# Performance work log

Measured on AMD Instinct MI355X. Metric: run time of the kernel, lower is better.

## Reference

```python
import jax, jax.numpy as jnp
import numpy as np

B, S, H = 2, 4096, 2048          # batch, seq_len, hidden_size
NH, D, W = 8, 128, 4             # num_kv_heads, head_dim, conv_kernel_size (window)
KD = NH * D                      # key_dim == value_dim == 1024
ROPE_BASE = 1000000.0
EPS = 1e-6


def _rope_tables(d, end, base):
    inv = 1.0 / (base ** (np.arange(0, d, 2)[: d // 2].astype(np.float32) / d))
    f = np.outer(np.arange(end, dtype=np.float32), inv)  # [end, d/2]
    return jnp.asarray(np.cos(f)), jnp.asarray(np.sin(f))


def _apply_rope(x, cos, sin):
    # x: [B,S,h,d]; llama-style interleaved pairs (2i, 2i+1)
    x0, x1 = x[..., 0::2], x[..., 1::2]
    c = cos[None, :, None, :]
    s = sin[None, :, None, :]
    o0 = x0 * c - x1 * s
    o1 = x0 * s + x1 * c
    return jnp.stack([o0, o1], axis=-1).reshape(x.shape)


def setup_inputs() -> dict:
    key = jax.random.key(0)
    ks = jax.random.split(key, 7)
    sd = lambda k, shape, fan_in: jax.random.normal(k, shape, jnp.float32) * (fan_in ** -0.5)
    return {
        "x": jax.random.normal(ks[0], (B, S, H), jnp.float32),
        "W_qkv": sd(ks[1], (H, 3 * KD), H),
        "W_z": sd(ks[2], (H, KD), H),
        "W_b": sd(ks[3], (H, NH), H),
        "W_a": sd(ks[4], (H, NH), H),
        "norm_w": jnp.ones((KD,), jnp.float32),
        "W_out": sd(ks[5], (KD, H), KD),
    }


def _forward(x, W_qkv, W_z, W_b, W_a, norm_w, W_out):
    cos, sin = _rope_tables(D, S, ROPE_BASE)
    qkv = x @ W_qkv
    q, k, v = qkv[..., :KD], qkv[..., KD:2 * KD], qkv[..., 2 * KD:]
    z = x @ W_z           # [B,S,KD]
    bg = x @ W_b          # [B,S,NH]
    ag = x @ W_a          # [B,S,NH]

    q4 = _apply_rope(q.reshape(B, S, NH, D), cos, sin)
    k4 = _apply_rope(k.reshape(B, S, NH, D), cos, sin)
    v4 = v.reshape(B, S, NH, D)

    # Windowed gated delta rule: out[i] = sum_{j=i-W..i} (q_i.k_j/sqrt(D)) * sigmoid(a_i*b_j) * v_j
    # Implemented per diagonal offset (W+1 small, fixed) -- never materializes an SxS matrix.
    scale = 1.0 / np.sqrt(D).astype(np.float32)
    out = jnp.zeros_like(v4)
    idx = jnp.arange(S)
    for off in range(W + 1):
        if off == 0:
            kj, vj, bj = k4, v4, bg
        else:
            kj = jnp.pad(k4, ((0, 0), (off, 0), (0, 0), (0, 0)))[:, :S]
            vj = jnp.pad(v4, ((0, 0), (off, 0), (0, 0), (0, 0)))[:, :S]
            bj = jnp.pad(bg, ((0, 0), (off, 0), (0, 0)))[:, :S]
        score = jnp.einsum('bshd,bshd->bsh', q4, kj) * scale
        s = score * jax.nn.sigmoid(ag * bj)
        s = jnp.where((idx >= off)[None, :, None], s, 0.0)
        out = out + s[..., None] * vj
    # position 0 bypasses the attention entirely: output[0] = v[0]
    out = out.at[:, 0].set(v4[:, 0])

    y = out.reshape(B, S, KD) * jax.nn.sigmoid(z)
    # GatedRMSNorm(y, z): rmsnorm(y) * weight * silu(z)
    yf = y.reshape(B * S, KD)
    zf = z.reshape(B * S, KD)
    rms = jnp.sqrt(jnp.mean(yf * yf, axis=-1, keepdims=True) + EPS)
    yn = (yf / rms) * norm_w * (zf * jax.nn.sigmoid(zf))
    return yn.reshape(B, S, KD) @ W_out


def reference(x, W_qkv, W_z, W_b, W_a, norm_w, W_out):
    return _forward(x, W_qkv, W_z, W_b, W_a, norm_w, W_out)
```

## Files before the change

kernel.cpp:

```cpp
#include <hip/hip_runtime.h>
#include <hip/hip_bf16.h>
#include <stdint.h>

#define B_   2
#define S_   4096
#define H_   2048
#define NH_  8
#define D_   128
#define KD_  1024
#define MR   (B_ * S_)
#define NQKVZ 4096

typedef __attribute__((ext_vector_type(8))) short bf16x8;
typedef __attribute__((ext_vector_type(4))) float f32x4;

__device__ __forceinline__ short f2bf(float f) {
    union { float f; uint32_t u; } v; v.f = f;
    uint32_t r = v.u + 0x7FFF + ((v.u >> 16) & 1);
    return (short)(r >> 16);
}
__device__ __forceinline__ float bf2f(unsigned short u) {
    union { uint32_t u; float f; } v; v.u = (uint32_t)u << 16; return v.f;
}

__device__ __forceinline__ void async_ld16(const void* g, void* l) {
    __builtin_amdgcn_global_load_lds(
        (const __attribute__((address_space(1))) uint32_t*)g,
        (__attribute__((address_space(3))) uint32_t*)l, 16, 0, 0);
}

__global__ __launch_bounds__(256) void k_wba(const float* __restrict__ Wb,
                                             const float* __restrict__ Wa,
                                             float* __restrict__ Wba) {
    int idx = blockIdx.x * 256 + threadIdx.x;
    int k = idx & 2047, c = idx >> 11;
    float v = (c < 8) ? Wb[(size_t)k * 8 + c] : Wa[(size_t)k * 8 + (c - 8)];
    Wba[(size_t)c * 2048 + k] = v;
}

__global__ __launch_bounds__(256) void k_cvt_bgag4(const float* __restrict__ x,
                                                   short* __restrict__ xb,
                                                   const float* __restrict__ Wba,
                                                   float* __restrict__ bgag) {
    const int m0 = blockIdx.x * 4, t = threadIdx.x;
    __shared__ float xs[4][2048];
    __shared__ float part[4][256];
#pragma unroll
    for (int rr = 0; rr < 4; rr++) {
        const float4* xr = (const float4*)(x + (size_t)(m0 + rr) * H_);
        float4 a = xr[t], b = xr[t + 256];
        ((float4*)xs[rr])[t] = a;
        ((float4*)xs[rr])[t + 256] = b;
        short4 oa, ob;
        oa.x = f2bf(a.x); oa.y = f2bf(a.y); oa.z = f2bf(a.z); oa.w = f2bf(a.w);
        ob.x = f2bf(b.x); ob.y = f2bf(b.y); ob.z = f2bf(b.z); ob.w = f2bf(b.w);
        short4* xo = (short4*)(xb + (size_t)(m0 + rr) * H_);
        xo[t] = oa;
        xo[t + 256] = ob;
    }
    __syncthreads();
    const int c = t & 15, seg = t >> 4;
    const int kb = seg * 128;
    const float4* W4 = (const float4*)(Wba + (size_t)c * 2048 + kb);
    const float4* x0 = (const float4*)&xs[0][kb];
    const float4* x1 = (const float4*)&xs[1][kb];
    const float4* x2 = (const float4*)&xs[2][kb];
    const float4* x3 = (const float4*)&xs[3][kb];
    float a0 = 0.f, a1 = 0.f, a2 = 0.f, a3 = 0.f;
#pragma unroll 8
    for (int k4 = 0; k4 < 32; k4++) {
        float4 w = W4[k4];
        float4 v0 = x0[k4], v1 = x1[k4], v2 = x2[k4], v3 = x3[k4];
        a0 += w.x * v0.x + w.y * v0.y + w.z * v0.z + w.w * v0.w;
        a1 += w.x * v1.x + w.y * v1.y + w.z * v1.z + w.w * v1.w;
        a2 += w.x * v2.x + w.y * v2.y + w.z * v2.z + w.w * v2.w;
        a3 += w.x * v3.x + w.y * v3.y + w.z * v3.z + w.w * v3.w;
    }
    part[0][t] = a0; part[1][t] = a1; part[2][t] = a2; part[3][t] = a3;
    __syncthreads();
    if (t < 64) {
        int rr = t >> 4, cc = t & 15;
        float s = 0.f;
#pragma unroll
        for (int j = 0; j < 16; j++) s += part[rr][j * 16 + cc];
        bgag[(size_t)(m0 + rr) * 16 + cc] = s;
    }
}

__global__ __launch_bounds__(256) void k_transpose_cvt(const float* __restrict__ W,
                                                       short* __restrict__ Wt,
                                                       int K, int N) {
    __shared__ float tile[32][33];
    int n0 = blockIdx.x * 32, k0 = blockIdx.y * 32;
    int tx = threadIdx.x, ty = threadIdx.y;
#pragma unroll
    for (int i = 0; i < 32; i += 8)
        tile[ty + i][tx] = W[(size_t)(k0 + ty + i) * N + n0 + tx];
    __syncthreads();
#pragma unroll
    for (int i = 0; i < 32; i += 8)
        Wt[(size_t)(n0 + ty + i) * K + k0 + tx] = f2bf(tile[tx][ty + i]);
}

__global__ __launch_bounds__(256) void k_ropetab(float2* __restrict__ ctab) {
    int idx = blockIdx.x * 256 + threadIdx.x;
    int i = idx & 63, s = idx >> 6;
    float inv = exp2f(-(float)i * (2.0f / 128.0f) * 19.931568569324174f);
    float f = (float)s * inv;
    float sn, cs;
    sincosf(f, &sn, &cs);
    ctab[idx] = make_float2(cs, sn);
}

#define PHASE_TAIL() \
    __builtin_amdgcn_s_setprio(0); \
    asm volatile("s_waitcnt vmcnt(%0)" :: "n"(2 + LB) : "memory"); \
    asm volatile("s_barrier" ::: "memory")
#define LDB_P(SET, BASE, KH) \
    _Pragma("unroll") for (int j = 0; j < NF; j++) \
        bf##SET[j] = *(const bf16x8*)((BASE) + 2 * AHB + (KH) * BHB + (wn + j * 16 + mrow) * 64 + kcA)
#define LDA03_P(SET, BASE, KH) \
    _Pragma("unroll") for (int i = 0; i < 4; i++) \
        af##SET[i] = *(const bf16x8*)((BASE) + (KH) * AHB + (wm + i * 16 + mrow) * 64 + kcA)
#define LDA47_S(BASE, KH) \
    _Pragma("unroll") for (int i = 0; i < 4; i++) \
        afS[i] = *(const bf16x8*)((BASE) + (KH) * AHB + (wm + 64 + i * 16 + mrow) * 64 + kcA)
#define MFMA_PH(SET) \
    _Pragma("unroll") for (int i = 0; i < 4; i++) \
    _Pragma("unroll") for (int j = 0; j < NF; j++) \
        acc[i][j] = __builtin_amdgcn_mfma_f32_16x16x32_bf16(af##SET[i], bf##SET[j], acc[i][j], 0, 0, 0); \
    _Pragma("unroll") for (int i = 0; i < 4; i++) \
    _Pragma("unroll") for (int j = 0; j < NF; j++) \
        acc[4 + i][j] = __builtin_amdgcn_mfma_f32_16x16x32_bf16(afS[i], bf##SET[j], acc[4 + i][j], 0, 0, 0)

template <int BN, int EPI>
__global__ __launch_bounds__(512, 2) void k_gemm256(const short* __restrict__ A,
                                                    const short* __restrict__ Bt,
                                                    float* __restrict__ Cf,
                                                    unsigned short* __restrict__ Cb,
                                                    const float2* __restrict__ ctab,
                                                    int M, int N, int K) {
    constexpr int BM = 256;
    constexpr int NF = BN / 64;
    constexpr int LB = BN / 128;
    constexpr int AHB = BM * 64;
    constexpr int BHB = BN * 64;
    constexpr int BUFB = 2 * AHB + 2 * BHB;
    constexpr int LDSB = (EPI == 0) ? 133120 : 2 * BUFB;
    __shared__ __align__(16) char lds[LDSB];

    const int t = threadIdx.x;
    const int lane = t & 63, wave = t >> 6;
    const int mrow = lane & 15;
    const int kcA = (((lane >> 4) ^ ((mrow >> 1) & 3)) * 16);

    const int nwg = gridDim.x;
    const int w0 = blockIdx.x;
    const int wg = (w0 & 7) * (nwg >> 3) + (w0 >> 3);
    const int NB = N / BN;
    const int bn = (wg % NB) * BN;
    const int bm = (wg / NB) * BM;

    const int wm = (wave >> 2) * 128;
    const int wn = (wave & 3) * (BN / 4);

    const short* __restrict__ Ab = A + (size_t)bm * K;
    const short* __restrict__ Bb = Bt + (size_t)bn * K;

    int aoff[2], adst[2];
#pragma unroll
    for (int l = 0; l < 2; l++) {
        int c = t + l * 512;
        int row = c >> 2;
        int kcg = (c & 3) ^ ((row >> 1) & 3);
        aoff[l] = row * K + kcg * 8;
        adst[l] = c * 16;
    }
    int boff[LB], bdst[LB];
#pragma unroll
    for (int l = 0; l < LB; l++) {
        int c = t + l * 512;
        int row = c >> 2;
        int kcg = (c & 3) ^ ((row >> 1) & 3);
        boff[l] = row * K + kcg * 8;
        bdst[l] = c * 16;
    }

    const int NT = K >> 6;

    auto stageA = [&](int kt, int kh, int p) {
        const short* g = Ab + kt * 64 + kh * 32;
        char* d = lds + p * BUFB + kh * AHB;
#pragma unroll
        for (int l = 0; l < 2; l++) async_ld16(g + aoff[l], d + adst[l]);
    };
    auto stageB = [&](int kt, int kh, int p) {
        const short* g = Bb + kt * 64 + kh * 32;
        char* d = lds + p * BUFB + 2 * AHB + kh * BHB;
#pragma unroll
        for (int l = 0; l < LB; l++) async_ld16(g + boff[l], d + bdst[l]);
    };

    f32x4 acc[8][NF] = {};
    bf16x8 afE[4], bfE[NF], afO[4], bfO[NF], afS[4];

    stageA(0, 0, 0); stageB(0, 0, 0);
    stageA(0, 1, 0); stageB(0, 1, 0);
    {
        int k1 = (NT > 1) ? 1 : 0;
        stageA(k1, 0, 1); stageB(k1, 0, 1);
    }
    asm volatile("s_waitcnt vmcnt(%0)" :: "n"(2 * (2 + LB)) : "memory");
    asm volatile("s_barrier" ::: "memory");
    LDB_P(E, lds, 0); LDA03_P(E, lds, 0);
    asm volatile("s_waitcnt vmcnt(%0)" :: "n"(2 + LB) : "memory");
    asm volatile("s_barrier" ::: "memory");

    for (int kt = 0; kt < NT; kt++) {
        const int p = kt & 1;
        const char* base = lds + p * BUFB;
        const char* baseN = lds + (p ^ 1) * BUFB;
        const int k1 = (kt + 1 < NT) ? (kt + 1) : (NT - 1);
        const int k2 = (kt + 2 < NT) ? (kt + 2) : (NT - 1);

        LDA47_S(base, 0);
        LDB_P(O, base, 1); LDA03_P(O, base, 1);
        stageA(k1, 1, p ^ 1); stageB(k1, 1, p ^ 1);
        __builtin_amdgcn_sched_barrier(0);
        __builtin_amdgcn_s_setprio(1);
        MFMA_PH(E);
        PHASE_TAIL();

        LDA47_S(base, 1);
        LDB_P(E, baseN, 0); LDA03_P(E, baseN, 0);
        stageA(k2, 0, p); stageB(k2, 0, p);
        __builtin_amdgcn_sched_barrier(0);
        __builtin_amdgcn_s_setprio(1);
        MFMA_PH(O);
        PHASE_TAIL();
    }
    asm volatile("s_waitcnt vmcnt(0)" ::: "memory");

    const int crow = (lane >> 4) * 4, ccol = lane & 15;
    if (EPI == 0) {
        float* lf = (float*)lds;
#pragma unroll
        for (int p2 = 0; p2 < 2; p2++) {
            __syncthreads();
#pragma unroll
            for (int i = 0; i < 4; i++) {
                const int ii = p2 * 4 + i;
#pragma unroll
                for (int j = 0; j < NF; j++)
#pragma unroll
                    for (int r = 0; r < 4; r++) {
                        int rl = wm + ii * 16 + crow + r;
                        int slot = (rl & 63) | ((rl >> 7) << 6);
                        lf[slot * 260 + wn + j * 16 + ccol] = acc[ii][j][r];
                    }
            }
            __syncthreads();
#pragma unroll
            for (int rep = 0; rep < 16; rep++) {
                int idx = rep * 512 + t;
                int slot = idx >> 6, c4 = idx & 63;
                int rl = (slot & 63) + p2 * 64 + ((slot >> 6) << 7);
                float4 v = *(const float4*)&lf[slot * 260 + c4 * 4];
                *(float4*)(Cf + (size_t)(bm + rl) * N + bn + c4 * 4) = v;
            }
        }
    } else {
#pragma unroll
        for (int i = 0; i < 8; i++)
#pragma unroll
            for (int j = 0; j < NF; j++) {
                const int col = bn + wn + j * 16 + ccol;
                const int rowb = bm + wm + i * 16 + crow;
                const bool qk = col < 2048;
                const int fi = (col & 127) >> 1;
                const bool even = (col & 1) == 0;
                uint32_t* Cd = (uint32_t*)(Cb + ((size_t)rowb * N + (col & ~1)));
#pragma unroll
                for (int r = 0; r < 4; r++) {
                    float v = acc[i][j][r];
                    if (qk) {
                        int s = (rowb + r) & (S_ - 1);
                        float2 cs = ctab[s * 64 + fi];
                        float pp = __shfl_xor(v, 1);
                        v = even ? v * cs.x - pp * cs.y : v * cs.x + pp * cs.y;
                    }
                    int hb = (int)(unsigned short)f2bf(v);
                    int pb = __shfl_xor(hb, 1);
                    if (even)
                        Cd[(size_t)r * (N >> 1)] = (uint32_t)(hb | (pb << 16));
                }
            }
    }
}

__global__ __launch_bounds__(256) void k_attn4(const unsigned short* __restrict__ qkvz,
                                               const float* __restrict__ bgag,
                                               const float* __restrict__ norm_w,
                                               short* __restrict__ yn) {
    const int m0 = blockIdx.x * 4;
    const int s0 = m0 & (S_ - 1);
    const int t = threadIdx.x;
    __shared__ unsigned short kvls[8][2048];
    __shared__ float sc[4][NH_][5];
    __shared__ float red[4][4];

#pragma unroll
    for (int i = 0; i < 8; i++) {
        int g = m0 - 4 + i;
        g = (g < 0) ? 0 : g;
        const uint4* src = (const uint4*)(qkvz + (size_t)g * NQKVZ + 1024);
        ((uint4*)kvls[i])[t] = src[t];
    }
    __syncthreads();

    {
        const int r = t >> 6, h = (t >> 3) & 7, l8 = t & 7;
        const int sr = s0 + r;
        const int nOff = (sr < 4 ? sr : 4) + 1;
        float qv[16];
        {
            const unsigned short* qg = qkvz + (size_t)(m0 + r) * NQKVZ + h * 128 + l8 * 16;
#pragma unroll
            for (int d = 0; d < 16; d++) qv[d] = bf2f(qg[d]);
        }
        const float ag = bgag[(size_t)(m0 + r) * 16 + 8 + h];
#pragma unroll
        for (int off = 0; off < 5; off++) {
            float acc = 0.f;
            const unsigned short* kk = kvls[r + 4 - off] + h * 128 + l8 * 16;
#pragma unroll
            for (int d = 0; d < 16; d++) acc += qv[d] * bf2f(kk[d]);
#pragma unroll
            for (int w = 1; w < 8; w <<= 1) acc += __shfl_xor(acc, w);
            if (l8 == 0) {
                float val = 0.f;
                if (off < nOff) {
                    float bg = bgag[(size_t)(m0 + r - off) * 16 + h];
                    float g = 1.f / (1.f + expf(-ag * bg));
                    val = acc * 0.08838834764831845f * g;
                }
                sc[r][h][off] = val;
            }
        }
    }
    __syncthreads();

    const int e0 = t * 4, h2 = t >> 5;
    float yv[4][4], zs[4][4], ssr[4];
    float nw[4];
    {
        const float4 n4 = *(const float4*)(norm_w + e0);
        nw[0] = n4.x; nw[1] = n4.y; nw[2] = n4.z; nw[3] = n4.w;
    }
#pragma unroll
    for (int r = 0; r < 4; r++) {
        const int sr = s0 + r;
        float o[4] = {0.f, 0.f, 0.f, 0.f};
        if (sr == 0) {
#pragma unroll
            for (int d = 0; d < 4; d++) o[d] = bf2f(kvls[r + 4][1024 + e0 + d]);
        } else {
            const int nOff = (sr < 4 ? sr : 4) + 1;
            for (int off = 0; off < nOff; off++) {
                float w = sc[r][h2][off];
#pragma unroll
                for (int d = 0; d < 4; d++)
                    o[d] += w * bf2f(kvls[r + 4 - off][1024 + e0 + d]);
            }
        }
        const unsigned short* zg = qkvz + (size_t)(m0 + r) * NQKVZ + 3072 + e0;
        float ss = 0.f;
#pragma unroll
        for (int d = 0; d < 4; d++) {
            float z = bf2f(zg[d]);
            float sg = 1.f / (1.f + expf(-z));
            yv[r][d] = o[d] * sg;
            zs[r][d] = z * sg;
            ss += yv[r][d] * yv[r][d];
        }
        ssr[r] = ss;
    }
    const int wave = t >> 6, lane = t & 63;
#pragma unroll
    for (int r = 0; r < 4; r++)
#pragma unroll
        for (int w = 1; w < 64; w <<= 1) ssr[r] += __shfl_xor(ssr[r], w);
    if (lane == 0) {
        red[wave][0] = ssr[0]; red[wave][1] = ssr[1];
        red[wave][2] = ssr[2]; red[wave][3] = ssr[3];
    }
    __syncthreads();
#pragma unroll
    for (int r = 0; r < 4; r++) {
        float tot = red[0][r] + red[1][r] + red[2][r] + red[3][r];
        float rinv = 1.f / sqrtf(tot * (1.0f / 1024.0f) + 1e-6f);
        short4 ov;
        ov.x = f2bf(yv[r][0] * rinv * nw[0] * zs[r][0]);
        ov.y = f2bf(yv[r][1] * rinv * nw[1] * zs[r][1]);
        ov.z = f2bf(yv[r][2] * rinv * nw[2] * zs[r][2]);
        ov.w = f2bf(yv[r][3] * rinv * nw[3] * zs[r][3]);
        ((short4*)yn)[(size_t)(m0 + r) * 256 + t] = ov;
    }
}

extern "C" void kernel_launch(void* const* d_in, const int* in_sizes, int n_in,
                              void* d_out, int out_size, void* d_ws, size_t ws_size,
                              hipStream_t stream) {
    const float* x      = (const float*)d_in[0];
    const float* W_qkv  = (const float*)d_in[1];
    const float* W_z    = (const float*)d_in[2];
    const float* W_b    = (const float*)d_in[3];
    const float* W_a    = (const float*)d_in[4];
    const float* norm_w = (const float*)d_in[5];
    const float* W_out  = (const float*)d_in[6];
    float* out = (float*)d_out;

    char* ws = (char*)d_ws;
    short* xb    = (short*)ws;          ws += (size_t)MR * H_ * 2;
    short* Wt1   = (short*)ws;          ws += (size_t)NQKVZ * H_ * 2;
    short* Wt2   = (short*)ws;          ws += (size_t)H_ * KD_ * 2;
    unsigned short* qkvzb = (unsigned short*)ws; ws += (size_t)MR * NQKVZ * 2;
    float* bgag  = (float*)ws;          ws += (size_t)MR * 16 * 4;
    short* yn    = (short*)ws;          ws += (size_t)MR * KD_ * 2;
    float2* ctab = (float2*)ws;         ws += (size_t)S_ * 64 * 8;
    float* Wba   = (float*)ws;          ws += (size_t)16 * 2048 * 4;

    k_wba<<<16 * 2048 / 256, 256, 0, stream>>>(W_b, W_a, Wba);
    k_cvt_bgag4<<<MR / 4, 256, 0, stream>>>(x, xb, Wba, bgag);
    k_transpose_cvt<<<dim3(3072 / 32, 2048 / 32), dim3(32, 8), 0, stream>>>(W_qkv, Wt1, 2048, 3072);
    k_transpose_cvt<<<dim3(1024 / 32, 2048 / 32), dim3(32, 8), 0, stream>>>(W_z, Wt1 + (size_t)3072 * 2048, 2048, 1024);
    k_transpose_cvt<<<dim3(2048 / 32, 1024 / 32), dim3(32, 8), 0, stream>>>(W_out, Wt2, 1024, 2048);
    k_ropetab<<<S_ * 64 / 256, 256, 0, stream>>>(ctab);
    k_gemm256<256, 1><<<(MR / 256) * (NQKVZ / 256), 512, 0, stream>>>(
        xb, Wt1, nullptr, qkvzb, ctab, MR, NQKVZ, H_);
    k_attn4<<<MR / 4, 256, 0, stream>>>(qkvzb, bgag, norm_w, yn);
    k_gemm256<256, 0><<<(MR / 256) * (H_ / 256), 512, 0, stream>>>(
        yn, Wt2, out, nullptr, nullptr, MR, H_, KD_);
}
```

Before: 440.1 us.

## Restructure GEMM main loop into eight-phase schedule with full-K tile swizzle

Replaces the two-phase GEMM loop with an eight-phase loop that processes two K-tiles per iteration. Each phase covers one quadrant of the wave's output tile. LDS is laid out as full 64-wide K rows with an 8-way XOR swizzle instead of two 32-wide halves. The A and B global-to-LDS stages are split across phases, with barriers and lgkm/vm waits placed around each MFMA block. The aim is better overlap of LDS reads, global prefetch and MFMA work. In exchange the kernel carries more barriers and more fragile waitcnt accounting.

Measured after the change: 436.7 us. About the same (-0.8%).

```diff
diff --git a/kernel.cpp b/kernel.cpp
--- a/kernel.cpp
+++ b/kernel.cpp
@@ -112,47 +112,55 @@
     ctab[idx] = make_float2(cs, sn);
 }
 
-#define PHASE_TAIL() \
+#define PH_BEGIN() \
+    asm volatile("s_barrier" ::: "memory"); \
+    asm volatile("s_waitcnt lgkmcnt(0)" ::: "memory"); \
+    __builtin_amdgcn_sched_barrier(0); \
+    __builtin_amdgcn_s_setprio(1)
+#define PH_END() \
     __builtin_amdgcn_s_setprio(0); \
-    asm volatile("s_waitcnt vmcnt(%0)" :: "n"(2 + LB) : "memory"); \
     asm volatile("s_barrier" ::: "memory")
-#define LDB_P(SET, BASE, KH) \
-    _Pragma("unroll") for (int j = 0; j < NF; j++) \
-        bf##SET[j] = *(const bf16x8*)((BASE) + 2 * AHB + (KH) * BHB + (wn + j * 16 + mrow) * 64 + kcA)
-#define LDA03_P(SET, BASE, KH) \
-    _Pragma("unroll") for (int i = 0; i < 4; i++) \
-        af##SET[i] = *(const bf16x8*)((BASE) + (KH) * AHB + (wm + i * 16 + mrow) * 64 + kcA)
-#define LDA47_S(BASE, KH) \
-    _Pragma("unroll") for (int i = 0; i < 4; i++) \
-        afS[i] = *(const bf16x8*)((BASE) + (KH) * AHB + (wm + 64 + i * 16 + mrow) * 64 + kcA)
-#define MFMA_PH(SET) \
-    _Pragma("unroll") for (int i = 0; i < 4; i++) \
-    _Pragma("unroll") for (int j = 0; j < NF; j++) \
-        acc[i][j] = __builtin_amdgcn_mfma_f32_16x16x32_bf16(af##SET[i], bf##SET[j], acc[i][j], 0, 0, 0); \
-    _Pragma("unroll") for (int i = 0; i < 4; i++) \
-    _Pragma("unroll") for (int j = 0; j < NF; j++) \
-        acc[4 + i][j] = __builtin_amdgcn_mfma_f32_16x16x32_bf16(afS[i], bf##SET[j], acc[4 + i][j], 0, 0, 0)
-
-template <int BN, int EPI>
-__global__ __launch_bounds__(512, 2) void k_gemm256(const short* __restrict__ A,
-                                                    const short* __restrict__ Bt,
-                                                    float* __restrict__ Cf,
-                                                    unsigned short* __restrict__ Cb,
-                                                    const float2* __restrict__ ctab,
-                                                    int M, int N, int K) {
-    constexpr int BM = 256;
-    constexpr int NF = BN / 64;
-    constexpr int LB = BN / 128;
-    constexpr int AHB = BM * 64;
-    constexpr int BHB = BN * 64;
-    constexpr int BUFB = 2 * AHB + 2 * BHB;
-    constexpr int LDSB = (EPI == 0) ? 133120 : 2 * BUFB;
+#define PH_END_V() \
+    __builtin_amdgcn_s_setprio(0); \
+    asm volatile("s_waitcnt vmcnt(4)" ::: "memory"); \
+    asm volatile("s_barrier" ::: "memory")
+#define RD_A(P, IH) \
+    _Pragma("unroll") for (int f = 0; f < 4; f++) { \
+        af[f][0] = *(const bf16x8*)(ArdB + (P) * BUF + (IH) * 8192 + f * 2048 + cb0); \
+        af[f][1] = *(const bf16x8*)(ArdB + (P) * BUF + (IH) * 8192 + f * 2048 + cb1); \
+    }
+#define RD_B(P, JH) \
+    _Pragma("unroll") for (int g = 0; g < 2; g++) { \
+        bf[g][0] = *(const bf16x8*)(BrdB + (P) * BUF + (JH) * 4096 + g * 2048 + cb0); \
+        bf[g][1] = *(const bf16x8*)(BrdB + (P) * BUF + (JH) * 4096 + g * 2048 + cb1); \
+    }
+#define MF(IH, JH) \
+    _Pragma("unroll") for (int f = 0; f < 4; f++) \
+    _Pragma("unroll") for (int g = 0; g < 2; g++) { \
+        acc[(IH) * 4 + f][(JH) * 2 + g] = __builtin_amdgcn_mfma_f32_16x16x32_bf16( \
+            af[f][0], bf[g][0], acc[(IH) * 4 + f][(JH) * 2 + g], 0, 0, 0); \
+        acc[(IH) * 4 + f][(JH) * 2 + g] = __builtin_amdgcn_mfma_f32_16x16x32_bf16( \
+            af[f][1], bf[g][1], acc[(IH) * 4 + f][(JH) * 2 + g], 0, 0, 0); \
+    }
+
+template <int EPI>
+__global__ __launch_bounds__(512, 2) void k_gemm8p(const short* __restrict__ A,
+                                                   const short* __restrict__ Bt,
+                                                   float* __restrict__ Cf,
+                                                   unsigned short* __restrict__ Cb,
+                                                   const float2* __restrict__ ctab,
+                                                   int M, int N, int K) {
+    constexpr int BM = 256, BN = 256;
+    constexpr int BUF = 65536, BOFF = 32768;
+    constexpr int LDSB = (EPI == 0) ? 133120 : 131072;
     __shared__ __align__(16) char lds[LDSB];
 
     const int t = threadIdx.x;
     const int lane = t & 63, wave = t >> 6;
-    const int mrow = lane & 15;
-    const int kcA = (((lane >> 4) ^ ((mrow >> 1) & 3)) * 16);
+    const int mrow = lane & 15, kq = lane >> 4;
+    const int fr = (mrow >> 1) & 7;
+    const int cb0 = (kq ^ fr) * 16;
+    const int cb1 = ((4 + kq) ^ fr) * 16;
 
     const int nwg = gridDim.x;
     const int w0 = blockIdx.x;
@@ -162,82 +170,70 @@
     const int bm = (wg / NB) * BM;
 
     const int wm = (wave >> 2) * 128;
-    const int wn = (wave & 3) * (BN / 4);
+    const int wn = (wave & 3) * 64;
 
     const short* __restrict__ Ab = A + (size_t)bm * K;
     const short* __restrict__ Bb = Bt + (size_t)bn * K;
 
-    int aoff[2], adst[2];
-#pragma unroll
-    for (int l = 0; l < 2; l++) {
-        int c = t + l * 512;
-        int row = c >> 2;
-        int kcg = (c & 3) ^ ((row >> 1) & 3);
-        aoff[l] = row * K + kcg * 8;
-        adst[l] = c * 16;
-    }
-    int boff[LB], bdst[LB];
-#pragma unroll
-    for (int l = 0; l < LB; l++) {
-        int c = t + l * 512;
-        int row = c >> 2;
-        int kcg = (c & 3) ^ ((row >> 1) & 3);
-        boff[l] = row * K + kcg * 8;
-        bdst[l] = c * 16;
-    }
+    const int uA = t >> 3, cA = t & 7;
+    const int swz = cA ^ ((uA >> 1) & 7);
+    size_t gq[4]; int lq[4];
+#pragma unroll
+    for (int q = 0; q < 4; q++) {
+        gq[q] = (size_t)(q * 64 + uA) * K + swz * 8;
+        lq[q] = (q * 64 + uA) * 128 + cA * 16;
+    }
+    auto stA02 = [&](int kt, int p) {
+        async_ld16(Ab + gq[0] + kt * 64, lds + p * BUF + lq[0]);
+        async_ld16(Ab + gq[2] + kt * 64, lds + p * BUF + lq[2]);
+    };
+    auto stA13 = [&](int kt, int p) {
+        async_ld16(Ab + gq[1] + kt * 64, lds + p * BUF + lq[1]);
+        async_ld16(Ab + gq[3] + kt * 64, lds + p * BUF + lq[3]);
+    };
+    auto stB = [&](int kt, int p) {
+#pragma unroll
+        for (int q = 0; q < 4; q++)
+            async_ld16(Bb + gq[q] + kt * 64, lds + p * BUF + BOFF + lq[q]);
+    };
+
+    const char* ArdB = lds + (wm + mrow) * 128;
+    const char* BrdB = lds + BOFF + (wn + mrow) * 128;
+
+    f32x4 acc[8][4] = {};
+    bf16x8 af[4][2], bf[2][2];
 
     const int NT = K >> 6;
 
-    auto stageA = [&](int kt, int kh, int p) {
-        const short* g = Ab + kt * 64 + kh * 32;
-        char* d = lds + p * BUFB + kh * AHB;
-#pragma unroll
-        for (int l = 0; l < 2; l++) async_ld16(g + aoff[l], d + adst[l]);
-    };
-    auto stageB = [&](int kt, int kh, int p) {
-        const short* g = Bb + kt * 64 + kh * 32;
-        char* d = lds + p * BUFB + 2 * AHB + kh * BHB;
-#pragma unroll
-        for (int l = 0; l < LB; l++) async_ld16(g + boff[l], d + bdst[l]);
-    };
-
-    f32x4 acc[8][NF] = {};
-    bf16x8 afE[4], bfE[NF], afO[4], bfO[NF], afS[4];
-
-    stageA(0, 0, 0); stageB(0, 0, 0);
-    stageA(0, 1, 0); stageB(0, 1, 0);
-    {
-        int k1 = (NT > 1) ? 1 : 0;
-        stageA(k1, 0, 1); stageB(k1, 0, 1);
-    }
-    asm volatile("s_waitcnt vmcnt(%0)" :: "n"(2 * (2 + LB)) : "memory");
+    stA02(0, 0); stA13(0, 0); stB(0, 0);
+    stA02(1, 1); stA13(1, 1);
+    asm volatile("s_waitcnt vmcnt(4)" ::: "memory");
     asm volatile("s_barrier" ::: "memory");
-    LDB_P(E, lds, 0); LDA03_P(E, lds, 0);
-    asm volatile("s_waitcnt vmcnt(%0)" :: "n"(2 + LB) : "memory");
-    asm volatile("s_barrier" ::: "memory");
-
-    for (int kt = 0; kt < NT; kt++) {
-        const int p = kt & 1;
-        const char* base = lds + p * BUFB;
-        const char* baseN = lds + (p ^ 1) * BUFB;
-        const int k1 = (kt + 1 < NT) ? (kt + 1) : (NT - 1);
-        const int k2 = (kt + 2 < NT) ? (kt + 2) : (NT - 1);
-
-        LDA47_S(base, 0);
-        LDB_P(O, base, 1); LDA03_P(O, base, 1);
-        stageA(k1, 1, p ^ 1); stageB(k1, 1, p ^ 1);
-        __builtin_amdgcn_sched_barrier(0);
-        __builtin_amdgcn_s_setprio(1);
-        MFMA_PH(E);
-        PHASE_TAIL();
-
-        LDA47_S(base, 1);
-        LDB_P(E, baseN, 0); LDA03_P(E, baseN, 0);
-        stageA(k2, 0, p); stageB(k2, 0, p);
-        __builtin_amdgcn_sched_barrier(0);
-        __builtin_amdgcn_s_setprio(1);
-        MFMA_PH(O);
-        PHASE_TAIL();
+
+    for (int it = 0; it < (NT >> 1); it++) {
+        const int kt1 = 2 * it + 1;
+        const int n0 = (2 * it + 2 < NT) ? 2 * it + 2 : NT - 1;
+        const int n1 = (2 * it + 3 < NT) ? 2 * it + 3 : NT - 1;
+
+        RD_A(0, 0); RD_B(0, 0); stB(kt1, 1);
+        asm volatile("s_waitcnt lgkmcnt(8)" ::: "memory");
+        PH_BEGIN(); MF(0, 0); PH_END();
+        RD_B(0, 1); stA02(n0, 0);
+        PH_BEGIN(); MF(0, 1); PH_END();
+        RD_A(0, 1);
+        PH_BEGIN(); MF(1, 1); PH_END();
+        RD_B(0, 0); stA13(n0, 0);
+        PH_BEGIN(); MF(1, 0); PH_END_V();
+
+        RD_A(1, 0); RD_B(1, 0); stB(n0, 0);
+        asm volatile("s_waitcnt lgkmcnt(8)" ::: "memory");
+        PH_BEGIN(); MF(0, 0); PH_END();
+        RD_B(1, 1);
+        PH_BEGIN(); MF(0, 1); PH_END();
+        RD_A(1, 1); stA02(n1, 1);
+        PH_BEGIN(); MF(1, 1); PH_END();
+        RD_B(1, 0); stA13(n1, 1);
+        PH_BEGIN(); MF(1, 0); PH_END_V();
     }
     asm volatile("s_waitcnt vmcnt(0)" ::: "memory");
 
@@ -251,7 +247,7 @@
             for (int i = 0; i < 4; i++) {
                 const int ii = p2 * 4 + i;
 #pragma unroll
-                for (int j = 0; j < NF; j++)
+                for (int j = 0; j < 4; j++)
 #pragma unroll
                     for (int r = 0; r < 4; r++) {
                         int rl = wm + ii * 16 + crow + r;
@@ -273,7 +269,7 @@
 #pragma unroll
         for (int i = 0; i < 8; i++)
 #pragma unroll
-            for (int j = 0; j < NF; j++) {
+            for (int j = 0; j < 4; j++) {
                 const int col = bn + wn + j * 16 + ccol;
                 const int rowb = bm + wm + i * 16 + crow;
                 const bool qk = col < 2048;
@@ -436,9 +432,9 @@
     k_transpose_cvt<<<dim3(1024 / 32, 2048 / 32), dim3(32, 8), 0, stream>>>(W_z, Wt1 + (size_t)3072 * 2048, 2048, 1024);
     k_transpose_cvt<<<dim3(2048 / 32, 1024 / 32), dim3(32, 8), 0, stream>>>(W_out, Wt2, 1024, 2048);
     k_ropetab<<<S_ * 64 / 256, 256, 0, stream>>>(ctab);
-    k_gemm256<256, 1><<<(MR / 256) * (NQKVZ / 256), 512, 0, stream>>>(
+    k_gemm8p<1><<<(MR / 256) * (NQKVZ / 256), 512, 0, stream>>>(
         xb, Wt1, nullptr, qkvzb, ctab, MR, NQKVZ, H_);
     k_attn4<<<MR / 4, 256, 0, stream>>>(qkvzb, bgag, norm_w, yn);
-    k_gemm256<256, 0><<<(MR / 256) * (H_ / 256), 512, 0, stream>>>(
+    k_gemm8p<0><<<(MR / 256) * (H_ / 256), 512, 0, stream>>>(
         yn, Wt2, out, nullptr, nullptr, MR, H_, KD_);
 }
```
